# Performance work log

Measured on AMD Instinct MI355X. Metric: run time of the kernel, lower is better.

## Reference

```python
import jax, jax.numpy as jnp
import numpy as np

K = 5  # kernel_size per dim, dim=2 -> 25 kernel weights, degree-1 open B-splines


def _spline_basis(pseudo):
    """Degree-1 open B-spline basis for dim=2, kernel_size=5.
    pseudo: [E,2] in [0,1]. Returns basis [E,4], kernel index wi [E,4]."""
    v = pseudo * (K - 1)                      # [E,2]
    lo = jnp.floor(v)
    frac = v - lo                             # [E,2]
    lo = lo.astype(jnp.int32)
    b = jnp.stack([1.0 - frac, frac], axis=-1)            # [E,2,2] (edge, dim, offset)
    idx = jnp.clip(lo[..., None] + jnp.arange(2, dtype=jnp.int32), 0, K - 1)  # [E,2,2]
    basis = b[:, 0, :, None] * b[:, 1, None, :]           # [E,2,2]
    wi = idx[:, 0, :, None] + K * idx[:, 1, None, :]      # [E,2,2] (dim0 stride 1, dim1 stride K)
    E = pseudo.shape[0]
    return basis.reshape(E, 4), wi.reshape(E, 4)


def _spline_conv(x, src, dst, pseudo, W, root, bias, num_nodes):
    basis, wi = _spline_basis(pseudo)          # [E,4], [E,4]
    xW = jnp.einsum('ni,kio->nko', x, W)       # [N,25,out]
    gathered = xW[src[:, None], wi]            # [E,4,out]
    msg = jnp.einsum('es,eso->eo', basis, gathered)  # [E,out]
    agg = jax.ops.segment_max(msg, dst, num_segments=num_nodes)
    agg = jnp.where(jnp.isneginf(agg), 0.0, agg)  # empty segments -> 0 (PyG fill)
    return agg + x @ root + bias


def setup_inputs() -> dict:
    key = jax.random.key(0)
    ks = jax.random.split(key, 12)
    N, E, C = 50000, 800000, 64
    s = 1.0 / np.sqrt(C)
    return {
        'x': jax.random.normal(ks[0], (N, C), jnp.float32),
        'edge_index': jax.random.randint(ks[1], (2, E), 0, N, jnp.int32),
        'edge_attr': jax.random.uniform(ks[2], (E, 2), jnp.float32),
        'W1': jax.random.normal(ks[3], (25, C, C), jnp.float32) * s,
        'root1': jax.random.normal(ks[4], (C, C), jnp.float32) * s,
        'b1': jnp.zeros((C,), jnp.float32),
        'W2': jax.random.normal(ks[5], (25, C, C), jnp.float32) * s,
        'root2': jax.random.normal(ks[6], (C, C), jnp.float32) * s,
        'b2': jnp.zeros((C,), jnp.float32),
        'final_w': jax.random.normal(ks[7], (3 * C, C), jnp.float32) / np.sqrt(3 * C),
        'final_b': jnp.zeros((C,), jnp.float32),
    }


def reference(x, edge_index, edge_attr, W1, root1, b1, W2, root2, b2, final_w, final_b):
    N = x.shape[0]
    src, dst = edge_index[0], edge_index[1]
    x1 = jax.nn.relu(_spline_conv(x, src, dst, edge_attr, W1, root1, b1, N))
    x2 = jax.nn.relu(_spline_conv(x1, src, dst, edge_attr, W2, root2, b2, N))
    h = jnp.concatenate([x, x1, x2], axis=-1)   # cat=True; dropout p=0 (eval)
    return h @ final_w + final_b
```

## Files before the change

kernel.cpp:

```cpp
#include <hip/hip_runtime.h>
#include <hip/hip_bf16.h>


typedef short  bf16x8 __attribute__((ext_vector_type(8)));
typedef float  f32x4  __attribute__((ext_vector_type(4)));

__device__ __forceinline__ float bf2f(ushort u) {
    return __uint_as_float((uint)u << 16);
}
__device__ __forceinline__ ushort f2bf(float f) {
    uint u = __float_as_uint(f);
    return (ushort)((u + 0x7FFF + ((u >> 16) & 1)) >> 16);
}

__global__ __launch_bounds__(256) void cvt_f32_bf16(
    const float* __restrict__ in, ushort* __restrict__ out, int n)
{
    int i = blockIdx.x * 256 + threadIdx.x;
    if (i < n) out[i] = f2bf(in[i]);
}

__global__ __launch_bounds__(256) void cvt_WT(
    const float* __restrict__ W, const float* __restrict__ root,
    ushort* __restrict__ Wt)
{
    int idx = blockIdx.x * 256 + threadIdx.x;
    if (idx >= 26 * 4096) return;
    int tile = idx >> 12, rem = idx & 4095, o = rem >> 6, i = rem & 63;
    float v = (tile < 25) ? W[tile * 4096 + i * 64 + o] : root[i * 64 + o];
    Wt[idx] = f2bf(v);
}

__global__ __launch_bounds__(256) void zero_ints(int* __restrict__ p, int n)
{
    int i = blockIdx.x * 256 + threadIdx.x;
    if (i < n) p[i] = 0;
}

__global__ __launch_bounds__(256) void hist_deg(
    const int* __restrict__ ei, int* __restrict__ deg, int E)
{
    int e = blockIdx.x * 256 + threadIdx.x;
    if (e < E) atomicAdd(&deg[ei[E + e]], 1);
}

__global__ __launch_bounds__(1024) void scan_block(
    const int* __restrict__ deg, int* __restrict__ inc,
    int* __restrict__ partial, int N)
{
    __shared__ int s[1024];
    int i = blockIdx.x * 1024 + threadIdx.x;
    int v = (i < N) ? deg[i] : 0;
    s[threadIdx.x] = v;
    __syncthreads();
    for (int off = 1; off < 1024; off <<= 1) {
        int t = (threadIdx.x >= off) ? s[threadIdx.x - off] : 0;
        __syncthreads();
        s[threadIdx.x] += t;
        __syncthreads();
    }
    if (i < N) inc[i] = s[threadIdx.x];
    if (threadIdx.x == 1023) partial[blockIdx.x] = s[1023];
}

__global__ void scan_partial(int* __restrict__ partial, int nb)
{
    __shared__ int s[64];
    int t = threadIdx.x;
    int v = (t < nb) ? partial[t] : 0;
    s[t] = v;
    __syncthreads();
    for (int off = 1; off < 64; off <<= 1) {
        int x = (t >= off) ? s[t - off] : 0;
        __syncthreads();
        s[t] += x;
        __syncthreads();
    }
    if (t < nb) partial[t] = s[t] - v;
}

__global__ __launch_bounds__(1024) void scan_finalize(
    const int* __restrict__ deg, const int* __restrict__ inc,
    const int* __restrict__ partial, int* __restrict__ row_ptr,
    int* __restrict__ cursor, int N)
{
    int i = blockIdx.x * 1024 + threadIdx.x;
    if (i >= N) return;
    int v = inc[i] + partial[blockIdx.x];
    row_ptr[i + 1] = v;
    cursor[i] = v - deg[i];
    if (i == 0) row_ptr[0] = 0;
}

__global__ __launch_bounds__(256) void csr_scatter(
    const int* __restrict__ ei, const float* __restrict__ attr,
    int* __restrict__ cursor, int4* __restrict__ epack, int E)
{
    int e = blockIdx.x * 256 + threadIdx.x;
    if (e >= E) return;
    int src = ei[e], dst = ei[E + e];
    float u = attr[2 * e] * 4.f;
    float v = attr[2 * e + 1] * 4.f;
    float lu = floorf(u), lv = floorf(v);
    float fu = u - lu, fv = v - lv;
    int iu = (int)lu;  iu = iu < 0 ? 0 : (iu > 4 ? 4 : iu);
    int iv = (int)lv;  iv = iv < 0 ? 0 : (iv > 4 ? 4 : iv);
    int iu1 = iu + 1 > 4 ? 4 : iu + 1;
    int iv1 = iv + 1 > 4 ? 4 : iv + 1;
    uint slots = (uint)(iu + 5 * iv) | ((uint)(iu + 5 * iv1) << 8) |
                 ((uint)(iu1 + 5 * iv) << 16) | ((uint)(iu1 + 5 * iv1) << 24);
    uint wlo = (uint)f2bf((1.f - fu) * (1.f - fv)) | ((uint)f2bf((1.f - fu) * fv) << 16);
    uint whi = (uint)f2bf(fu * (1.f - fv)) | ((uint)f2bf(fu * fv) << 16);
    int pos = atomicAdd(&cursor[dst], 1);
    epack[pos] = make_int4(src * 3200, (int)slots, (int)wlo, (int)whi);
}

__global__ __launch_bounds__(256) void gemm_xw(
    const ushort* __restrict__ A, const ushort* __restrict__ Wt,
    ushort* __restrict__ xWb, float* __restrict__ xRoot, int mtiles)
{
    __shared__ ushort Cs[64][72];
    const int bx = blockIdx.x;
    const int wave = threadIdx.x >> 6;
    const int lane = threadIdx.x & 63;
    const int l16 = lane & 15;
    const int half = lane >> 4;
    const int tid = threadIdx.x;

    const ushort* btile = Wt + (size_t)bx * 4096;
    bf16x8 b0[4], b1[4];
    #pragma unroll
    for (int s = 0; s < 4; ++s) {
        const ushort* brow = btile + (size_t)(s * 16 + l16) * 64;
        b0[s] = *(const bf16x8*)(brow + half * 8);
        b1[s] = *(const bf16x8*)(brow + 32 + half * 8);
    }

    for (int it = 0; it < 8; ++it) {
        const int mt = blockIdx.y * 8 + it;
        if (mt >= mtiles) break;
        const int m0 = mt * 64;
        const int m_base = m0 + wave * 16;

        const ushort* arow = A + (size_t)(m_base + l16) * 64;
        bf16x8 a0 = *(const bf16x8*)(arow + half * 8);
        bf16x8 a1 = *(const bf16x8*)(arow + 32 + half * 8);

        f32x4 acc[4];
        #pragma unroll
        for (int s = 0; s < 4; ++s) {
            acc[s] = (f32x4){0.f, 0.f, 0.f, 0.f};
            acc[s] = __builtin_amdgcn_mfma_f32_16x16x32_bf16(a0, b0[s], acc[s], 0, 0, 0);
            acc[s] = __builtin_amdgcn_mfma_f32_16x16x32_bf16(a1, b1[s], acc[s], 0, 0, 0);
        }

        if (bx == 25) {
            #pragma unroll
            for (int s = 0; s < 4; ++s)
                #pragma unroll
                for (int r = 0; r < 4; ++r)
                    xRoot[(size_t)(m_base + half * 4 + r) * 64 + s * 16 + l16] = acc[s][r];
            continue;
        }

        #pragma unroll
        for (int s = 0; s < 4; ++s)
            #pragma unroll
            for (int r = 0; r < 4; ++r)
                Cs[wave * 16 + half * 4 + r][s * 16 + l16] = f2bf(acc[s][r]);
        __syncthreads();
        #pragma unroll
        for (int i2 = 0; i2 < 2; ++i2) {
            int idx = tid + i2 * 256;
            int row = idx >> 3, seg = idx & 7;
            uint4 v = *(const uint4*)&Cs[row][seg * 8];
            *(uint4*)(xWb + (size_t)(m0 + row) * 1600 + bx * 64 + seg * 8) = v;
        }
        __syncthreads();
    }
}

__device__ __forceinline__ void gather4(
    const char* __restrict__ xwb, int lane, int rb, uint slots, ushort g[4])
{
    g[0] = *((const ushort*)(xwb + rb + ((slots & 255u) << 7)) + lane);
    g[1] = *((const ushort*)(xwb + rb + (((slots >> 8) & 255u) << 7)) + lane);
    g[2] = *((const ushort*)(xwb + rb + (((slots >> 16) & 255u) << 7)) + lane);
    g[3] = *((const ushort*)(xwb + rb + ((slots >> 24) << 7)) + lane);
}

__device__ __forceinline__ float consume4(const int4 d, const ushort g[4])
{
    float m = __uint_as_float((uint)d.z << 16) * bf2f(g[0]);
    m = fmaf(__uint_as_float((uint)d.z & 0xffff0000u), bf2f(g[1]), m);
    m = fmaf(__uint_as_float((uint)d.w << 16), bf2f(g[2]), m);
    m = fmaf(__uint_as_float((uint)d.w & 0xffff0000u), bf2f(g[3]), m);
    return m;
}

__global__ __launch_bounds__(256) void edge_csr(
    const ushort* __restrict__ xWb, const int* __restrict__ row_ptr,
    const int4* __restrict__ epack, const float* __restrict__ xRoot,
    const float* __restrict__ bias, float* __restrict__ outf,
    ushort* __restrict__ outb, int N)
{
    const int wv = __builtin_amdgcn_readfirstlane(threadIdx.x >> 6);
    const int d = blockIdx.x * 4 + wv;
    const int lane = threadIdx.x & 63;
    if (d >= N) return;
    const int e0 = __builtin_amdgcn_readfirstlane(row_ptr[d]);
    const int e1 = __builtin_amdgcn_readfirstlane(row_ptr[d + 1]);
    const char* xwb = (const char*)xWb;

    float vmax = -__builtin_inff();
    int e = e0;
    const int pairs = (e1 - e0) >> 1;
    if (pairs > 0) {
        int4 dA = epack[e], dB = epack[e + 1];
        ushort gA[4], gB[4];
        gather4(xwb, lane, dA.x, (uint)dA.y, gA);
        gather4(xwb, lane, dB.x, (uint)dB.y, gB);
        for (int p = 1; p < pairs; ++p) {
            int4 nA = epack[e + 2 * p], nB = epack[e + 2 * p + 1];
            ushort hA[4], hB[4];
            gather4(xwb, lane, nA.x, (uint)nA.y, hA);
            gather4(xwb, lane, nB.x, (uint)nB.y, hB);
            vmax = fmaxf(vmax, fmaxf(consume4(dA, gA), consume4(dB, gB)));
            #pragma unroll
            for (int i = 0; i < 4; ++i) { gA[i] = hA[i]; gB[i] = hB[i]; }
            dA = nA; dB = nB;
        }
        vmax = fmaxf(vmax, fmaxf(consume4(dA, gA), consume4(dB, gB)));
        e += pairs * 2;
    }
    if (e < e1) {
        int4 dA = epack[e];
        ushort gA[4];
        gather4(xwb, lane, dA.x, (uint)dA.y, gA);
        vmax = fmaxf(vmax, consume4(dA, gA));
    }
    if (e1 == e0) vmax = 0.f;
    float val = vmax + xRoot[(size_t)d * 64 + lane] + bias[lane];
    val = fmaxf(val, 0.f);
    outf[(size_t)d * 64 + lane] = val;
    if (outb) outb[(size_t)d * 64 + lane] = f2bf(val);
}

__global__ __launch_bounds__(256) void final_gemm(
    const float* __restrict__ x, const float* __restrict__ x1,
    const float* __restrict__ x2, const float* __restrict__ fw,
    const float* __restrict__ fb, float* __restrict__ out, int M)
{
    __shared__ float As[64][68];
    __shared__ float Bs[64][68];
    const int m0 = blockIdx.x * 64;
    const int tid = threadIdx.x;
    const int tx = tid & 15, ty = tid >> 4;
    float acc[4][4] = {};
    const float* srcs[3] = {x, x1, x2};

    for (int kt = 0; kt < 3; ++kt) {
        const float* A = srcs[kt];
        const float4* B4 = (const float4*)(fw + (size_t)kt * 4096);
        #pragma unroll
        for (int r = 0; r < 4; ++r) {
            int idx = tid + r * 256;
            float4 v = B4[idx];
            int i = idx >> 4;
            int o = (idx & 15) * 4;
            Bs[i][o] = v.x; Bs[i][o + 1] = v.y; Bs[i][o + 2] = v.z; Bs[i][o + 3] = v.w;
        }
        #pragma unroll
        for (int r = 0; r < 4; ++r) {
            int idx = tid + r * 256;
            int m = idx >> 4;
            int k = (idx & 15) * 4;
            int gm = m0 + m;
            float4 v = make_float4(0.f, 0.f, 0.f, 0.f);
            if (gm < M) v = *(const float4*)(A + (size_t)gm * 64 + k);
            As[k][m] = v.x; As[k + 1][m] = v.y; As[k + 2][m] = v.z; As[k + 3][m] = v.w;
        }
        __syncthreads();
        #pragma unroll 8
        for (int k = 0; k < 64; ++k) {
            float4 av = *(const float4*)&As[k][ty * 4];
            float4 bv = *(const float4*)&Bs[k][tx * 4];
            float aa[4] = {av.x, av.y, av.z, av.w};
            float bb[4] = {bv.x, bv.y, bv.z, bv.w};
            #pragma unroll
            for (int i = 0; i < 4; ++i)
                #pragma unroll
                for (int j = 0; j < 4; ++j)
                    acc[i][j] = fmaf(aa[i], bb[j], acc[i][j]);
        }
        __syncthreads();
    }

    #pragma unroll
    for (int i = 0; i < 4; ++i) {
        int gm = m0 + ty * 4 + i;
        if (gm < M) {
            float4 v = make_float4(acc[i][0] + fb[tx * 4 + 0],
                                   acc[i][1] + fb[tx * 4 + 1],
                                   acc[i][2] + fb[tx * 4 + 2],
                                   acc[i][3] + fb[tx * 4 + 3]);
            *(float4*)(out + (size_t)gm * 64 + tx * 4) = v;
        }
    }
}

extern "C" void kernel_launch(void* const* d_in, const int* in_sizes, int n_in,
                              void* d_out, int out_size, void* d_ws, size_t ws_size,
                              hipStream_t stream)
{
    const float* x    = (const float*)d_in[0];
    const int*   ei   = (const int*)d_in[1];
    const float* attr = (const float*)d_in[2];
    const float* W1   = (const float*)d_in[3];
    const float* r1   = (const float*)d_in[4];
    const float* b1   = (const float*)d_in[5];
    const float* W2   = (const float*)d_in[6];
    const float* r2   = (const float*)d_in[7];
    const float* b2   = (const float*)d_in[8];
    const float* fw   = (const float*)d_in[9];
    const float* fb   = (const float*)d_in[10];
    float* out = (float*)d_out;

    const int N = in_sizes[0] / 64;
    const int E = in_sizes[1] / 2;
    const int mtiles = (N + 63) / 64;
    const int Npad = mtiles * 64;

    char* p = (char*)d_ws;
    auto alloc = [&](size_t bytes) { void* q = p; p += (bytes + 255) & ~(size_t)255; return q; };
    int4*   epack  = (int4*)alloc((size_t)E * 16);
    float*  x1f    = (float*)alloc((size_t)Npad * 64 * 4);
    float*  x2f    = (float*)alloc((size_t)Npad * 64 * 4);
    float*  xRoot  = (float*)alloc((size_t)Npad * 64 * 4);
    ushort* xWb    = (ushort*)alloc((size_t)Npad * 1600 * 2);
    ushort* xb     = (ushort*)alloc((size_t)Npad * 64 * 2);
    ushort* x1b    = (ushort*)alloc((size_t)Npad * 64 * 2);
    ushort* WtA    = (ushort*)alloc((size_t)26 * 4096 * 2);
    ushort* WtB    = (ushort*)alloc((size_t)26 * 4096 * 2);
    int*    deg    = (int*)alloc((size_t)N * 4);
    int*    cursor = (int*)alloc((size_t)N * 4);
    int*    rowp   = (int*)alloc((size_t)(N + 1) * 4);
    int*    tmpinc = (int*)alloc((size_t)N * 4);
    int*    part   = (int*)alloc(64 * 4);

    const int nb = (N + 1023) / 1024;

    cvt_f32_bf16<<<(N * 64 + 255) / 256, 256, 0, stream>>>(x, xb, N * 64);
    cvt_WT<<<(26 * 4096 + 255) / 256, 256, 0, stream>>>(W1, r1, WtA);
    cvt_WT<<<(26 * 4096 + 255) / 256, 256, 0, stream>>>(W2, r2, WtB);

    zero_ints<<<(N + 255) / 256, 256, 0, stream>>>(deg, N);
    hist_deg<<<(E + 255) / 256, 256, 0, stream>>>(ei, deg, E);
    scan_block<<<nb, 1024, 0, stream>>>(deg, tmpinc, part, N);
    scan_partial<<<1, 64, 0, stream>>>(part, nb);
    scan_finalize<<<nb, 1024, 0, stream>>>(deg, tmpinc, part, rowp, cursor, N);
    csr_scatter<<<(E + 255) / 256, 256, 0, stream>>>(ei, attr, cursor, epack, E);

    const dim3 ggrid(26, (mtiles + 7) / 8);

    gemm_xw<<<ggrid, 256, 0, stream>>>(xb, WtA, xWb, xRoot, mtiles);
    edge_csr<<<(N + 3) / 4, 256, 0, stream>>>(xWb, rowp, epack, xRoot, b1, x1f, x1b, N);

    gemm_xw<<<ggrid, 256, 0, stream>>>(x1b, WtB, xWb, xRoot, mtiles);
    edge_csr<<<(N + 3) / 4, 256, 0, stream>>>(xWb, rowp, epack, xRoot, b2, x2f, nullptr, N);

    final_gemm<<<mtiles, 256, 0, stream>>>(x, x1f, x2f, fw, fb, out, N);
}
```

Baseline: 428.4 us.

## Split xW table into two source-row halves so gather working set fits cache

The xW gemm and the edge gather now run in two passes over source-node halves. Each pass computes xW only for one half of the nodes into a buffer half the size. The edge kernel filters edges by source range, and the first pass stores a partial max to a float buffer that the second pass merges. The aim is a smaller random-gather working set that stays cache-resident (roughly 80MB per half instead of 160MB). In exchange every edge's metadata is read twice, there are extra launches, and a full-size float partial-max buffer is written and read back. The old software-pipelined gather loop is replaced with a simple per-edge loop.

```diff
diff --git a/kernel.cpp b/kernel.cpp
--- a/kernel.cpp
+++ b/kernel.cpp
@@ -180,27 +180,11 @@
     }
 }
 
-__device__ __forceinline__ void gather4(
-    const char* __restrict__ xwb, int lane, int rb, uint slots, ushort g[4])
-{
-    g[0] = *((const ushort*)(xwb + rb + ((slots & 255u) << 7)) + lane);
-    g[1] = *((const ushort*)(xwb + rb + (((slots >> 8) & 255u) << 7)) + lane);
-    g[2] = *((const ushort*)(xwb + rb + (((slots >> 16) & 255u) << 7)) + lane);
-    g[3] = *((const ushort*)(xwb + rb + ((slots >> 24) << 7)) + lane);
-}
-
-__device__ __forceinline__ float consume4(const int4 d, const ushort g[4])
-{
-    float m = __uint_as_float((uint)d.z << 16) * bf2f(g[0]);
-    m = fmaf(__uint_as_float((uint)d.z & 0xffff0000u), bf2f(g[1]), m);
-    m = fmaf(__uint_as_float((uint)d.w << 16), bf2f(g[2]), m);
-    m = fmaf(__uint_as_float((uint)d.w & 0xffff0000u), bf2f(g[3]), m);
-    return m;
-}
-
+template<int PHASE>
 __global__ __launch_bounds__(256) void edge_csr(
-    const ushort* __restrict__ xWb, const int* __restrict__ row_ptr,
-    const int4* __restrict__ epack, const float* __restrict__ xRoot,
+    const ushort* __restrict__ xWc, const int* __restrict__ row_ptr,
+    const int4* __restrict__ epack, int rb_base, int rb_len,
+    float* __restrict__ aggf, const float* __restrict__ xRoot,
     const float* __restrict__ bias, float* __restrict__ outf,
     ushort* __restrict__ outb, int N)
 {
@@ -210,36 +194,33 @@
     if (d >= N) return;
     const int e0 = __builtin_amdgcn_readfirstlane(row_ptr[d]);
     const int e1 = __builtin_amdgcn_readfirstlane(row_ptr[d + 1]);
-    const char* xwb = (const char*)xWb;
+    const char* xwb = (const char*)xWc;
+    const int lane2 = lane * 2;
 
     float vmax = -__builtin_inff();
-    int e = e0;
-    const int pairs = (e1 - e0) >> 1;
-    if (pairs > 0) {
-        int4 dA = epack[e], dB = epack[e + 1];
-        ushort gA[4], gB[4];
-        gather4(xwb, lane, dA.x, (uint)dA.y, gA);
-        gather4(xwb, lane, dB.x, (uint)dB.y, gB);
-        for (int p = 1; p < pairs; ++p) {
-            int4 nA = epack[e + 2 * p], nB = epack[e + 2 * p + 1];
-            ushort hA[4], hB[4];
-            gather4(xwb, lane, nA.x, (uint)nA.y, hA);
-            gather4(xwb, lane, nB.x, (uint)nB.y, hB);
-            vmax = fmaxf(vmax, fmaxf(consume4(dA, gA), consume4(dB, gB)));
-            #pragma unroll
-            for (int i = 0; i < 4; ++i) { gA[i] = hA[i]; gB[i] = hB[i]; }
-            dA = nA; dB = nB;
-        }
-        vmax = fmaxf(vmax, fmaxf(consume4(dA, gA), consume4(dB, gB)));
-        e += pairs * 2;
-    }
-    if (e < e1) {
-        int4 dA = epack[e];
-        ushort gA[4];
-        gather4(xwb, lane, dA.x, (uint)dA.y, gA);
-        vmax = fmaxf(vmax, consume4(dA, gA));
-    }
-    if (e1 == e0) vmax = 0.f;
+    for (int e = e0; e < e1; ++e) {
+        int4 de = epack[e];
+        int rel = de.x - rb_base;
+        if ((uint)rel >= (uint)rb_len) continue;
+        uint slots = (uint)de.y;
+        const char* base = xwb + rel + lane2;
+        float m = __uint_as_float((uint)de.z << 16) *
+                  bf2f(*(const ushort*)(base + ((slots & 255u) << 7)));
+        m = fmaf(__uint_as_float((uint)de.z & 0xffff0000u),
+                 bf2f(*(const ushort*)(base + (((slots >> 8) & 255u) << 7))), m);
+        m = fmaf(__uint_as_float((uint)de.w << 16),
+                 bf2f(*(const ushort*)(base + (((slots >> 16) & 255u) << 7))), m);
+        m = fmaf(__uint_as_float((uint)de.w & 0xffff0000u),
+                 bf2f(*(const ushort*)(base + ((slots >> 24) << 7))), m);
+        vmax = fmaxf(vmax, m);
+    }
+
+    if (PHASE == 0) {
+        aggf[(size_t)d * 64 + lane] = vmax;
+        return;
+    }
+    vmax = fmaxf(vmax, aggf[(size_t)d * 64 + lane]);
+    if (vmax == -__builtin_inff()) vmax = 0.f;
     float val = vmax + xRoot[(size_t)d * 64 + lane] + bias[lane];
     val = fmaxf(val, 0.f);
     outf[(size_t)d * 64 + lane] = val;
@@ -331,13 +312,18 @@
     const int mtiles = (N + 63) / 64;
     const int Npad = mtiles * 64;
 
+    const int mt0c = (mtiles + 1) / 2;
+    const int mt1c = mtiles - mt0c;
+    const int rows0 = mt0c * 64;
+
     char* p = (char*)d_ws;
     auto alloc = [&](size_t bytes) { void* q = p; p += (bytes + 255) & ~(size_t)255; return q; };
     int4*   epack  = (int4*)alloc((size_t)E * 16);
     float*  x1f    = (float*)alloc((size_t)Npad * 64 * 4);
     float*  x2f    = (float*)alloc((size_t)Npad * 64 * 4);
     float*  xRoot  = (float*)alloc((size_t)Npad * 64 * 4);
-    ushort* xWb    = (ushort*)alloc((size_t)Npad * 1600 * 2);
+    float*  aggf   = (float*)alloc((size_t)Npad * 64 * 4);
+    ushort* xWb    = (ushort*)alloc((size_t)rows0 * 1600 * 2);
     ushort* xb     = (ushort*)alloc((size_t)Npad * 64 * 2);
     ushort* x1b    = (ushort*)alloc((size_t)Npad * 64 * 2);
     ushort* WtA    = (ushort*)alloc((size_t)26 * 4096 * 2);
@@ -361,13 +347,26 @@
     scan_finalize<<<nb, 1024, 0, stream>>>(deg, tmpinc, part, rowp, cursor, N);
     csr_scatter<<<(E + 255) / 256, 256, 0, stream>>>(ei, attr, cursor, epack, E);
 
-    const dim3 ggrid(26, (mtiles + 7) / 8);
-
-    gemm_xw<<<ggrid, 256, 0, stream>>>(xb, WtA, xWb, xRoot, mtiles);
-    edge_csr<<<(N + 3) / 4, 256, 0, stream>>>(xWb, rowp, epack, xRoot, b1, x1f, x1b, N);
-
-    gemm_xw<<<ggrid, 256, 0, stream>>>(x1b, WtB, xWb, xRoot, mtiles);
-    edge_csr<<<(N + 3) / 4, 256, 0, stream>>>(xWb, rowp, epack, xRoot, b2, x2f, nullptr, N);
+    const int egrid = (N + 3) / 4;
+    const ushort* Ws[2] = {WtA, WtB};
+    const float*  bs[2] = {b1, b2};
+    const ushort* xin[2] = {xb, x1b};
+    float*  outF[2] = {x1f, x2f};
+    ushort* outB[2] = {x1b, nullptr};
+
+    for (int layer = 0; layer < 2; ++layer) {
+        gemm_xw<<<dim3(26, (mt0c + 7) / 8), 256, 0, stream>>>(
+            xin[layer], Ws[layer], xWb, xRoot, mt0c);
+        edge_csr<0><<<egrid, 256, 0, stream>>>(
+            xWb, rowp, epack, 0, rows0 * 3200,
+            aggf, xRoot, bs[layer], nullptr, nullptr, N);
+        gemm_xw<<<dim3(26, (mt1c + 7) / 8), 256, 0, stream>>>(
+            xin[layer] + (size_t)rows0 * 64, Ws[layer], xWb,
+            xRoot + (size_t)rows0 * 64, mt1c);
+        edge_csr<1><<<egrid, 256, 0, stream>>>(
+            xWb, rowp, epack, rows0 * 3200, mt1c * 64 * 3200,
+            aggf, xRoot, bs[layer], outF[layer], outB[layer], N);
+    }
 
     final_gemm<<<mtiles, 256, 0, stream>>>(x, x1f, x2f, fw, fb, out, N);
 }
```

After: 514.5 us. 20.1% more time.
